# Kernel tuning notes

Measured on AMD Instinct MI355X. Metric: run time of the kernel, lower is better.

Reference implementation:

```python
import jax, jax.numpy as jnp
import numpy as np

NUM_GENES = 4384
D_MODEL = 128


def setup_inputs() -> dict:
    key = jax.random.key(0)
    ks = jax.random.split(key, 8)
    B = 8
    return {
        "mutation_input": jax.random.normal(ks[0], (B, NUM_GENES, 4), dtype=jnp.float32),
        "external_V": jax.random.normal(ks[1], (NUM_GENES, D_MODEL), dtype=jnp.float32),
        "W_in": jax.random.normal(ks[2], (4, D_MODEL), dtype=jnp.float32) * 0.5,
        "b_in": jnp.zeros((D_MODEL,), dtype=jnp.float32),
        "key_param": jax.random.normal(ks[3], (NUM_GENES, D_MODEL), dtype=jnp.float32),
        "W1": jax.random.normal(ks[4], (D_MODEL, 64), dtype=jnp.float32) * (1.0 / np.sqrt(D_MODEL)),
        "b1": jnp.zeros((64,), dtype=jnp.float32),
        "W2": jax.random.normal(ks[5], (64, 26), dtype=jnp.float32) * 0.125,
        "b2": jnp.zeros((26,), dtype=jnp.float32),
    }


def reference(mutation_input, external_V, W_in, b_in, key_param, W1, b1, W2, b2):
    # Q: [B, G, D]
    Q = jnp.einsum("bgf,fd->bgd", mutation_input, W_in) + b_in
    scale = 1.0 / jnp.sqrt(jnp.asarray(Q.shape[-1], Q.dtype))
    # scores: [B, G, G] -- full matrix as in the original module
    scores = jnp.einsum("bqd,kd->bqk", Q, key_param) * scale
    attn = jax.nn.softmax(scores, axis=-1)
    # attention output: [B, G, D]
    attn_out = jnp.einsum("bqk,kd->bqd", attn, external_V)
    mean_out = attn_out.mean(axis=1)  # [B, D]
    h = jax.nn.gelu(mean_out @ W1 + b1, approximate=False)
    out = h @ W2 + b2  # [B, 26]
    return out
```

## Files before the change

### kernel.cpp

```cpp
#include <hip/hip_runtime.h>
#include <hip/hip_bf16.h>

#define NUM_GENES 4384
#define GPAD 4608
#define DM 128
#define ROWB 256
#define LDS_STRIDE 272
#define NTILES 137
#define RB_BLOCKS 18
#define NCHUNK 12
#define TPC 12

typedef __attribute__((ext_vector_type(8))) short short8;
typedef __attribute__((ext_vector_type(16))) float floatx16;

#if defined(__has_builtin)
#  if __has_builtin(__builtin_amdgcn_exp2f)
#    define FAST_EXP2(x) __builtin_amdgcn_exp2f(x)
#  endif
#endif
#ifndef FAST_EXP2
#  define FAST_EXP2(x) exp2f(x)
#endif

__global__ __launch_bounds__(256)
void prep_all(const float* __restrict__ mut, const float* __restrict__ W_in,
              const float* __restrict__ b_in, const float* __restrict__ key,
              __hip_bfloat16* __restrict__ Qb, __hip_bfloat16* __restrict__ Kb,
              float* __restrict__ l, float* __restrict__ w, float* __restrict__ meanbuf) {
    int bx = blockIdx.x, t = threadIdx.x;
    if (bx < 18432) {
        int idx = bx * 256 + t;
        int d = idx & 127;
        int g = (idx >> 7) % GPAD;
        int b = idx / (GPAD * 128);
        float v = 0.f;
        if (g < NUM_GENES) {
            const float* m = mut + ((size_t)b * NUM_GENES + g) * 4;
            v = b_in[d] + m[0] * W_in[d] + m[1] * W_in[128 + d]
                        + m[2] * W_in[256 + d] + m[3] * W_in[384 + d];
            v *= (0.08838834764831845f * 1.4426950408889634f);
        }
        Qb[idx] = __float2bfloat16(v);
    } else if (bx < 20736) {
        int idx = (bx - 18432) * 256 + t;
        int g = idx >> 7;
        float v = (g < NUM_GENES) ? key[idx] : 0.f;
        Kb[idx] = __float2bfloat16(v);
    } else {
        int i = (bx - 20736) * 256 + t;
        l[i] = 0.f;
        w[i] = 0.f;
        if (i < 1024) meanbuf[i] = 0.f;
    }
}

template <bool PB>
__global__ __launch_bounds__(256)
void phase_kernel(const __hip_bfloat16* __restrict__ Qb,
                  const __hip_bfloat16* __restrict__ Kb,
                  const float* __restrict__ lsum,
                  float* __restrict__ out) {
    __shared__ __align__(16) char tile[2][32 * LDS_STRIDE];

    int rb    = blockIdx.x;
    int chunk = blockIdx.y;
    int b     = blockIdx.z;

    const char* resident = (const char*)(PB ? Kb : (Qb + (size_t)b * GPAD * DM));
    const char* stream   = (const char*)(PB ? (Qb + (size_t)b * GPAD * DM) : Kb);

    int t = threadIdx.x;
    int lane = t & 63, wid = t >> 6;
    int m = lane & 31, half = lane >> 5;

    short8 afrag[2][8];
#pragma unroll
    for (int g = 0; g < 2; ++g) {
        const char* arow = resident + (size_t)(rb * 256 + wid * 64 + g * 32 + m) * ROWB;
#pragma unroll
        for (int dsl = 0; dsl < 8; ++dsl)
            afrag[g][dsl] = *(const short8*)(arow + dsl * 32 + half * 16);
    }

    float lacc[2][16];
#pragma unroll
    for (int g = 0; g < 2; ++g)
#pragma unroll
        for (int r = 0; r < 16; ++r) lacc[g][r] = 0.f;

    int t0 = chunk * TPC;
    int t1 = min(NTILES, t0 + TPC);
    int sr = t >> 3, sc = t & 7;
    int soff = sr * LDS_STRIDE + sc * 32;

    {
        const char* src = stream + (size_t)(t0 * 32 + sr) * ROWB + sc * 32;
        float4 v0 = *(const float4*)src;
        float4 v1 = *(const float4*)(src + 16);
        *(float4*)(tile[0] + soff) = v0;
        *(float4*)(tile[0] + soff + 16) = v1;
    }

    int p = 0;
    for (int kt = t0; kt < t1; ++kt) {
        bool more = (kt + 1 < t1);
        float4 v0, v1;
        if (more) {
            const char* s2 = stream + (size_t)((kt + 1) * 32 + sr) * ROWB + sc * 32;
            v0 = *(const float4*)s2;
            v1 = *(const float4*)(s2 + 16);
        }
        __syncthreads();

        floatx16 acc0, acc1;
#pragma unroll
        for (int r = 0; r < 16; ++r) { acc0[r] = 0.f; acc1[r] = 0.f; }
#pragma unroll
        for (int dsl = 0; dsl < 8; ++dsl) {
            short8 bfrag = *(const short8*)(tile[p] + m * LDS_STRIDE + dsl * 32 + half * 16);
            acc0 = __builtin_amdgcn_mfma_f32_32x32x16_bf16(afrag[0][dsl], bfrag, acc0, 0, 0, 0);
            acc1 = __builtin_amdgcn_mfma_f32_32x32x16_bf16(afrag[1][dsl], bfrag, acc1, 0, 0, 0);
        }

        if (more) {
            *(float4*)(tile[p ^ 1] + soff) = v0;
            *(float4*)(tile[p ^ 1] + soff + 16) = v1;
        }

        if (PB) {
            float scl = 1.0f / lsum[b * GPAD + kt * 32 + m];
#pragma unroll
            for (int r = 0; r < 16; ++r) {
                lacc[0][r] = fmaf(FAST_EXP2(acc0[r]), scl, lacc[0][r]);
                lacc[1][r] = fmaf(FAST_EXP2(acc1[r]), scl, lacc[1][r]);
            }
        } else {
#pragma unroll
            for (int r = 0; r < 16; ++r) {
                lacc[0][r] += FAST_EXP2(acc0[r]);
                lacc[1][r] += FAST_EXP2(acc1[r]);
            }
        }
        p ^= 1;
    }

#pragma unroll
    for (int off = 1; off <= 16; off <<= 1)
#pragma unroll
        for (int g = 0; g < 2; ++g)
#pragma unroll
            for (int r = 0; r < 16; ++r)
                lacc[g][r] += __shfl_xor(lacc[g][r], off, 64);

    if (m == 0) {
#pragma unroll
        for (int g = 0; g < 2; ++g) {
            float* ob = out + b * GPAD + rb * 256 + wid * 64 + g * 32 + 4 * half;
#pragma unroll
            for (int r = 0; r < 16; ++r)
                atomicAdd(ob + (r & 3) + 8 * (r >> 2), lacc[g][r]);
        }
    }
}

__global__ __launch_bounds__(256)
void mean_k(const float* __restrict__ w, const float* __restrict__ V,
            float* __restrict__ meanbuf) {
    int rb = blockIdx.x, b = blockIdx.y;
    int t = threadIdx.x;
    int d = t & 127, half = t >> 7;
    int g0 = rb * 128 + half * 64;
    int nv = NUM_GENES - g0;
    if (nv > 64) nv = 64;
    float a = 0.f;
    if (nv > 0) {
        const float* wb = w + b * GPAD + g0;
        const float* Vp = V + (size_t)g0 * 128 + d;
        for (int k = 0; k < nv; ++k)
            a += wb[k] * Vp[(size_t)k * 128];
    }
    atomicAdd(meanbuf + b * 128 + d, a);
}

__global__ void mlp_k(const float* __restrict__ meanbuf,
                      const float* __restrict__ W1, const float* __restrict__ b1,
                      const float* __restrict__ W2, const float* __restrict__ b2,
                      float* __restrict__ out) {
    int b = blockIdx.x, t = threadIdx.x;
    __shared__ float sh[64];
    const float* mb = meanbuf + b * 128;
    float s = b1[t];
    for (int d = 0; d < 128; ++d)
        s += (mb[d] * (1.0f / 4384.0f)) * W1[d * 64 + t];
    sh[t] = 0.5f * s * (1.0f + erff(s * 0.70710678118654752f));
    __syncthreads();
    if (t < 26) {
        float o = b2[t];
        for (int j = 0; j < 64; ++j) o += sh[j] * W2[j * 26 + t];
        out[b * 26 + t] = o;
    }
}

extern "C" void kernel_launch(void* const* d_in, const int* in_sizes, int n_in,
                              void* d_out, int out_size, void* d_ws, size_t ws_size,
                              hipStream_t stream) {
    const float* mut  = (const float*)d_in[0];
    const float* V    = (const float*)d_in[1];
    const float* W_in = (const float*)d_in[2];
    const float* b_in = (const float*)d_in[3];
    const float* key  = (const float*)d_in[4];
    const float* W1   = (const float*)d_in[5];
    const float* b1   = (const float*)d_in[6];
    const float* W2   = (const float*)d_in[7];
    const float* b2   = (const float*)d_in[8];
    float* out = (float*)d_out;

    char* ws = (char*)d_ws;
    __hip_bfloat16* Qb = (__hip_bfloat16*)(ws);
    __hip_bfloat16* Kb = (__hip_bfloat16*)(ws + 9437184);
    float* lbuf        = (float*)(ws + 10616832);
    float* wbuf        = (float*)(ws + 10764288);
    float* meanbuf     = (float*)(ws + 10911744);

    prep_all<<<20880, 256, 0, stream>>>(mut, W_in, b_in, key, Qb, Kb, lbuf, wbuf, meanbuf);

    dim3 grid(RB_BLOCKS, NCHUNK, 8);
    phase_kernel<false><<<grid, 256, 0, stream>>>(Qb, Kb, lbuf, lbuf);
    phase_kernel<true><<<grid, 256, 0, stream>>>(Qb, Kb, lbuf, wbuf);

    mean_k<<<dim3(35, 8), 256, 0, stream>>>(wbuf, V, meanbuf);
    mlp_k<<<8, 64, 0, stream>>>(meanbuf, W1, b1, W2, b2, out);
}
```

Baseline: 243.7 us.

## Vectorize prep kernel to 8 elements per thread and halve chunk count

```diff
diff --git a/kernel.cpp b/kernel.cpp
--- a/kernel.cpp
+++ b/kernel.cpp
@@ -8,8 +8,8 @@
 #define LDS_STRIDE 272
 #define NTILES 137
 #define RB_BLOCKS 18
-#define NCHUNK 12
-#define TPC 12
+#define NCHUNK 6
+#define TPC 23
 
 typedef __attribute__((ext_vector_type(8))) short short8;
 typedef __attribute__((ext_vector_type(16))) float floatx16;
@@ -23,35 +23,65 @@
 #  define FAST_EXP2(x) exp2f(x)
 #endif
 
+static __device__ __forceinline__ short bf16bits(float x) {
+    __hip_bfloat16 h = __float2bfloat16(x);
+    return *(short*)&h;
+}
+
 __global__ __launch_bounds__(256)
 void prep_all(const float* __restrict__ mut, const float* __restrict__ W_in,
               const float* __restrict__ b_in, const float* __restrict__ key,
               __hip_bfloat16* __restrict__ Qb, __hip_bfloat16* __restrict__ Kb,
               float* __restrict__ l, float* __restrict__ w, float* __restrict__ meanbuf) {
     int bx = blockIdx.x, t = threadIdx.x;
-    if (bx < 18432) {
-        int idx = bx * 256 + t;
-        int d = idx & 127;
-        int g = (idx >> 7) % GPAD;
-        int b = idx / (GPAD * 128);
-        float v = 0.f;
+    if (bx < 2304) {
+        int i = bx * 256 + t;
+        int d0 = (i & 15) * 8;
+        int g = (i >> 4) % GPAD;
+        int b = i / (GPAD * 16);
+        short8 o;
         if (g < NUM_GENES) {
-            const float* m = mut + ((size_t)b * NUM_GENES + g) * 4;
-            v = b_in[d] + m[0] * W_in[d] + m[1] * W_in[128 + d]
-                        + m[2] * W_in[256 + d] + m[3] * W_in[384 + d];
-            v *= (0.08838834764831845f * 1.4426950408889634f);
-        }
-        Qb[idx] = __float2bfloat16(v);
-    } else if (bx < 20736) {
-        int idx = (bx - 18432) * 256 + t;
-        int g = idx >> 7;
-        float v = (g < NUM_GENES) ? key[idx] : 0.f;
-        Kb[idx] = __float2bfloat16(v);
+            const float4 mv = *(const float4*)(mut + ((size_t)b * NUM_GENES + g) * 4);
+            const float sc = 0.08838834764831845f * 1.4426950408889634f;
+#pragma unroll
+            for (int j = 0; j < 8; ++j) {
+                int d = d0 + j;
+                float v = b_in[d] + mv.x * W_in[d] + mv.y * W_in[128 + d]
+                                  + mv.z * W_in[256 + d] + mv.w * W_in[384 + d];
+                o[j] = bf16bits(v * sc);
+            }
+        } else {
+#pragma unroll
+            for (int j = 0; j < 8; ++j) o[j] = 0;
+        }
+        *(short8*)((short*)Qb + (size_t)i * 8) = o;
+    } else if (bx < 2592) {
+        int i = (bx - 2304) * 256 + t;
+        int g = i >> 4;
+        short8 o;
+        if (g < NUM_GENES) {
+            const float4 k0 = *(const float4*)(key + (size_t)i * 8);
+            const float4 k1 = *(const float4*)(key + (size_t)i * 8 + 4);
+            o[0] = bf16bits(k0.x); o[1] = bf16bits(k0.y);
+            o[2] = bf16bits(k0.z); o[3] = bf16bits(k0.w);
+            o[4] = bf16bits(k1.x); o[5] = bf16bits(k1.y);
+            o[6] = bf16bits(k1.z); o[7] = bf16bits(k1.w);
+        } else {
+#pragma unroll
+            for (int j = 0; j < 8; ++j) o[j] = 0;
+        }
+        *(short8*)((short*)Kb + (size_t)i * 8) = o;
     } else {
-        int i = (bx - 20736) * 256 + t;
-        l[i] = 0.f;
-        w[i] = 0.f;
-        if (i < 1024) meanbuf[i] = 0.f;
+        int i = (bx - 2592) * 256 + t;
+        float4 z = {0.f, 0.f, 0.f, 0.f};
+        *(float4*)(l + (size_t)i * 8) = z;
+        *(float4*)(l + (size_t)i * 8 + 4) = z;
+        *(float4*)(w + (size_t)i * 8) = z;
+        *(float4*)(w + (size_t)i * 8 + 4) = z;
+        if (bx == 2592 && t < 128) {
+            *(float4*)(meanbuf + t * 8) = z;
+            *(float4*)(meanbuf + t * 8 + 4) = z;
+        }
     }
 }
 
@@ -223,7 +253,7 @@
     float* wbuf        = (float*)(ws + 10764288);
     float* meanbuf     = (float*)(ws + 10911744);
 
-    prep_all<<<20880, 256, 0, stream>>>(mut, W_in, b_in, key, Qb, Kb, lbuf, wbuf, meanbuf);
+    prep_all<<<2610, 256, 0, stream>>>(mut, W_in, b_in, key, Qb, Kb, lbuf, wbuf, meanbuf);
 
     dim3 grid(RB_BLOCKS, NCHUNK, 8);
     phase_kernel<false><<<grid, 256, 0, stream>>>(Qb, Kb, lbuf, lbuf);
```

New measurement: 212.0 us. 13.0% less time.
